# Kernel optimization log

Measured on AMD Instinct MI355X. Metric: run time of the kernel, lower is better.

The kernel has to match this reference:

```python
import jax, jax.numpy as jnp
import numpy as np

N = 100000        # nodes
E = 1600000       # edges (avg degree 16)
F_IN = 64         # num_node_features
NHID = 64         # args.nhid
NCLS = 16         # num_classes
K1 = 8            # Chebyshev order of conv1


def setup_inputs() -> dict:
    key = jax.random.key(0)
    k0, k1, k2, k3 = jax.random.split(key, 4)
    x = jax.random.normal(k0, (N, F_IN), dtype=jnp.float32)
    edge_index = jax.random.randint(k1, (2, E), 0, N, dtype=jnp.int32)
    # ChebConv params: K linear maps (no per-lin bias) + one shared bias
    W1 = jax.random.normal(k2, (K1, F_IN, NHID), dtype=jnp.float32) * (1.0 / np.sqrt(F_IN))
    b1 = jnp.zeros((NHID,), dtype=jnp.float32)
    W2 = jax.random.normal(k3, (1, NHID, NCLS), dtype=jnp.float32) * (1.0 / np.sqrt(NHID))
    b2 = jnp.zeros((NCLS,), dtype=jnp.float32)
    return {"x": x, "edge_index": edge_index, "W1": W1, "b1": b1, "W2": W2, "b2": b2}


def _cheb_norm(edge_index, num_nodes):
    # PyG ChebConv.__norm__ with normalization='sym', lambda_max=2.0, unit edge weights:
    # remove self loops; L_hat = 2L/lambda_max - I = -D^{-1/2} A D^{-1/2}, diag = 0.
    row, col = edge_index[0], edge_index[1]
    nonself = (row != col).astype(jnp.float32)
    deg = jax.ops.segment_sum(nonself, row, num_segments=num_nodes)
    dinv = jnp.where(deg > 0, jax.lax.rsqrt(jnp.maximum(deg, 1.0)), 0.0)
    norm = -dinv[row] * dinv[col] * nonself
    return row, col, norm


def reference(x, edge_index, W1, b1, W2, b2):
    row, col, norm = _cheb_norm(edge_index, N)

    def prop(h):  # L_hat @ h via gather + scatter-add, [N,F]
        return jax.ops.segment_sum(h[col] * norm[:, None], row, num_segments=N)

    # conv1: ChebConv K=8 recursion  Tx_k = 2*L_hat*Tx_{k-1} - Tx_{k-2}
    tx_prev = x
    out = x @ W1[0]
    tx = prop(x)
    out = out + tx @ W1[1]
    for k in range(2, K1):
        tx_new = 2.0 * prop(tx) - tx_prev
        out = out + tx_new @ W1[k]
        tx_prev, tx = tx, tx_new
    h = jax.nn.relu(out + b1)
    # dropout: identity (eval mode)
    # conv2: ChebConv K=1 -> just Tx_0 = h
    logits = h @ W2[0] + b2
    return jax.nn.softmax(logits, axis=1)
```

## Files before the change

kernel.cpp:

```cpp
#include <hip/hip_runtime.h>
#include <hip/hip_fp16.h>

#define N_NODES 100000
#define N_EDGES 1600000
#define F 64
#define NCLS 16
#define K1 8
#define BSH 9
#define NBK 196
#define BROWS 512
#define BKCAP 9216
#define EPB 4096

using f16x8 = __attribute__((ext_vector_type(8))) _Float16;
using f32x4 = __attribute__((ext_vector_type(4))) float;

__global__ __launch_bounds__(256) void k_bucketA(const int* __restrict__ ei,
                                                 int* __restrict__ gcur,
                                                 int2* __restrict__ bk) {
    __shared__ int cnt[4][256];
    __shared__ int wbase[4][256];
    int tid = threadIdx.x;
    int w = tid >> 6;
    for (int i = tid; i < 1024; i += 256) ((int*)cnt)[i] = 0;
    __syncthreads();
    int packed[16];
    int e0 = blockIdx.x * EPB;
#pragma unroll
    for (int u = 0; u < 16; u++) {
        int e = e0 + u * 256 + tid;
        packed[u] = -1;
        if (e < N_EDGES) {
            int r = ei[e], c = ei[N_EDGES + e];
            if (r != c) {
                int b = r >> BSH;
                int rank = atomicAdd(&cnt[w][b], 1);
                packed[u] = (rank << 8) | b;
            }
        }
    }
    __syncthreads();
    {
        int c0 = cnt[0][tid], c1 = cnt[1][tid], c2 = cnt[2][tid], c3 = cnt[3][tid];
        int tot = c0 + c1 + c2 + c3;
        int g = tot ? atomicAdd(&gcur[tid], tot) : 0;
        wbase[0][tid] = g;
        wbase[1][tid] = g + c0;
        wbase[2][tid] = g + c0 + c1;
        wbase[3][tid] = g + c0 + c1 + c2;
    }
    __syncthreads();
#pragma unroll
    for (int u = 0; u < 16; u++) {
        if (packed[u] >= 0) {
            int e = e0 + u * 256 + tid;
            int r = ei[e], c = ei[N_EDGES + e];
            int b = packed[u] & 255;
            int rank = packed[u] >> 8;
            bk[(size_t)b * BKCAP + wbase[w][b] + rank] = make_int2(r, c);
        }
    }
}

__global__ __launch_bounds__(256) void k_degB(const int2* __restrict__ bk,
                                              const int* __restrict__ gcur,
                                              int* __restrict__ deg,
                                              float* __restrict__ dinv) {
    __shared__ int hist[BROWS];
    int b = blockIdx.x;
    for (int i = threadIdx.x; i < BROWS; i += 256) hist[i] = 0;
    __syncthreads();
    int cnt = gcur[b];
    const int2* src = bk + (size_t)b * BKCAP;
    for (int i = threadIdx.x; i < cnt; i += 256)
        atomicAdd(&hist[src[i].x & (BROWS - 1)], 1);
    __syncthreads();
    int rbase = b << BSH;
    for (int i = threadIdx.x; i < BROWS; i += 256) {
        int gr = rbase + i;
        if (gr < N_NODES) {
            int d = hist[i];
            deg[gr] = d;
            dinv[gr] = d > 0 ? rsqrtf((float)d) : 0.f;
        }
    }
}

__global__ void k_scan1(const int* __restrict__ deg, int* __restrict__ rowptr, int* __restrict__ bsum) {
    __shared__ int sd[256];
    int tid = threadIdx.x;
    int base = blockIdx.x * 1024 + tid * 4;
    int v[4];
#pragma unroll
    for (int j = 0; j < 4; j++) {
        int idx = base + j;
        v[j] = (idx < N_NODES) ? deg[idx] : 0;
    }
    int s = v[0] + v[1] + v[2] + v[3];
    sd[tid] = s;
    __syncthreads();
    for (int d = 1; d < 256; d <<= 1) {
        int t = (tid >= d) ? sd[tid - d] : 0;
        __syncthreads();
        sd[tid] += t;
        __syncthreads();
    }
    int excl = sd[tid] - s;
    if (tid == 255) bsum[blockIdx.x] = sd[255];
    int run = excl;
#pragma unroll
    for (int j = 0; j < 4; j++) {
        int idx = base + j;
        if (idx < N_NODES) rowptr[idx] = run;
        run += v[j];
    }
}

__global__ void k_scan2(int* __restrict__ bsum, int* __restrict__ rowptr, int nblk) {
    if (threadIdx.x == 0 && blockIdx.x == 0) {
        int acc = 0;
        for (int b = 0; b < nblk; b++) { int t = bsum[b]; bsum[b] = acc; acc += t; }
        rowptr[N_NODES] = acc;
    }
}

__global__ void k_scan3(int* __restrict__ rowptr, const int* __restrict__ bsum) {
    int tid = threadIdx.x;
    int base = blockIdx.x * 1024 + tid * 4;
    int off = bsum[blockIdx.x];
#pragma unroll
    for (int j = 0; j < 4; j++) {
        int idx = base + j;
        if (idx < N_NODES) rowptr[idx] += off;
    }
}

__global__ __launch_bounds__(256) void k_fillB(const int2* __restrict__ bk,
                                               const int* __restrict__ gcur,
                                               const int* __restrict__ rowptr,
                                               const float* __restrict__ dinv,
                                               int2* __restrict__ csr_ew) {
    __shared__ int cur[BROWS];
    int b = blockIdx.x;
    for (int i = threadIdx.x; i < BROWS; i += 256) cur[i] = 0;
    __syncthreads();
    int cnt = gcur[b];
    const int2* src = bk + (size_t)b * BKCAP;
    for (int i = threadIdx.x; i < cnt; i += 256) {
        int2 rc = src[i];
        int rank = atomicAdd(&cur[rc.x & (BROWS - 1)], 1);
        float w = -dinv[rc.x] * dinv[rc.y];
        csr_ew[rowptr[rc.x] + rank] = make_int2(rc.y, __float_as_int(w));
    }
}

__global__ void k_cvt(const float* __restrict__ x, __half* __restrict__ t0) {
    int i = blockIdx.x * blockDim.x + threadIdx.x;
    int base = i * 4;
    if (base >= N_NODES * F) return;
    float4 v = *(const float4*)&x[base];
    __half2 a = __floats2half2_rn(v.x, v.y);
    __half2 b = __floats2half2_rn(v.z, v.w);
    *(__half2*)&t0[base] = a;
    *(__half2*)&t0[base + 2] = b;
}

__global__ void k_prepW(const float* __restrict__ W1, __half* __restrict__ Wf) {
    int t = blockIdx.x * blockDim.x + threadIdx.x;
    if (t >= K1 * 2 * 4 * 64) return;
    int lane = t & 63;
    int cb = (t >> 6) & 3;
    int fg = (t >> 8) & 1;
    int kidx = t >> 9;
    int col = cb * 16 + (lane & 15);
    int kbase = fg * 32 + (lane >> 4) * 8;
    f16x8 v;
#pragma unroll
    for (int j = 0; j < 8; j++)
        v[j] = (_Float16)W1[kidx * 4096 + (kbase + j) * 64 + col];
    *(f16x8*)(Wf + (size_t)t * 8) = v;
}

__global__ __launch_bounds__(256) void k_prop(const int* __restrict__ rowptr,
                                              const int2* __restrict__ csr_ew,
                                              const __half* __restrict__ src,
                                              const __half* __restrict__ prev,
                                              __half* __restrict__ dst,
                                              float alpha, float beta) {
    int wpair = (int)((blockIdx.x * blockDim.x + threadIdx.x) >> 6);
    int lane = threadIdx.x & 63;
    int nA = wpair * 2;
    if (nA >= N_NODES) return;
    int h = lane >> 5;
    int hl = lane & 31;
    int s3 = (lane >> 3) & 3;
    int fb = (lane & 7) * 8;
    int node = nA + h;
    bool valid = node < N_NODES;
    int cb  = valid ? rowptr[node] : 0;
    int end = valid ? rowptr[node + 1] : 0;

    float acc[8] = {};

    while (true) {
        int n_own = end - cb;
        if (n_own > 32) n_own = 32;
        if (n_own < 0) n_own = 0;
        int n_oth = __shfl(n_own, lane ^ 32, 64);
        int nmax = n_own > n_oth ? n_own : n_oth;
        if (nmax == 0) break;
        int2 e = make_int2(0, 0);
        if (hl < n_own) e = csr_ew[cb + hl];
        for (int j = 0; j < nmax; j += 16) {
            int cc[4];
            float ww[4];
#pragma unroll
            for (int g = 0; g < 4; g++) {
                int sl = (h << 5) | (j + g * 4 + s3);
                cc[g] = __shfl(e.x, sl, 64);
                ww[g] = __int_as_float(__shfl(e.y, sl, 64));
            }
            uint4 raw[4];
#pragma unroll
            for (int g = 0; g < 4; g++)
                raw[g] = *(const uint4*)(src + (size_t)cc[g] * F + fb);
#pragma unroll
            for (int g = 0; g < 4; g++) {
                float2 f0 = __half22float2(*(__half2*)&raw[g].x);
                float2 f1 = __half22float2(*(__half2*)&raw[g].y);
                float2 f2 = __half22float2(*(__half2*)&raw[g].z);
                float2 f3 = __half22float2(*(__half2*)&raw[g].w);
                acc[0] = fmaf(ww[g], f0.x, acc[0]);
                acc[1] = fmaf(ww[g], f0.y, acc[1]);
                acc[2] = fmaf(ww[g], f1.x, acc[2]);
                acc[3] = fmaf(ww[g], f1.y, acc[3]);
                acc[4] = fmaf(ww[g], f2.x, acc[4]);
                acc[5] = fmaf(ww[g], f2.y, acc[5]);
                acc[6] = fmaf(ww[g], f3.x, acc[6]);
                acc[7] = fmaf(ww[g], f3.y, acc[7]);
            }
        }
        cb += n_own;
    }

#pragma unroll
    for (int i = 0; i < 8; i++) {
        acc[i] += __shfl_xor(acc[i], 8, 64);
        acc[i] += __shfl_xor(acc[i], 16, 64);
    }

    if ((lane & 24) == 0 && valid) {
        float r[8];
#pragma unroll
        for (int i = 0; i < 8; i++) r[i] = alpha * acc[i];
        if (beta != 0.f) {
            uint4 pv = *(const uint4*)(prev + (size_t)node * F + fb);
            float2 p0 = __half22float2(*(__half2*)&pv.x);
            float2 p1 = __half22float2(*(__half2*)&pv.y);
            float2 p2 = __half22float2(*(__half2*)&pv.z);
            float2 p3 = __half22float2(*(__half2*)&pv.w);
            r[0] -= beta * p0.x; r[1] -= beta * p0.y;
            r[2] -= beta * p1.x; r[3] -= beta * p1.y;
            r[4] -= beta * p2.x; r[5] -= beta * p2.y;
            r[6] -= beta * p3.x; r[7] -= beta * p3.y;
        }
        uint4 outv;
        *(__half2*)&outv.x = __floats2half2_rn(r[0], r[1]);
        *(__half2*)&outv.y = __floats2half2_rn(r[2], r[3]);
        *(__half2*)&outv.z = __floats2half2_rn(r[4], r[5]);
        *(__half2*)&outv.w = __floats2half2_rn(r[6], r[7]);
        *(uint4*)(dst + (size_t)node * F + fb) = outv;
    }
}

__global__ __launch_bounds__(256) void k_fused_mfma(const __half* __restrict__ T,
                                                    const __half* __restrict__ Wf,
                                                    const float* __restrict__ b1,
                                                    const float* __restrict__ W2,
                                                    const float* __restrict__ b2,
                                                    float* __restrict__ y) {
    __shared__ float Ht[64][65];
    __shared__ float W2l[64 * 16];
    __shared__ float b2l[16];
    int tid = threadIdx.x;
    int lane = tid & 63;
    int w = tid >> 6;
    int ln15 = lane & 15;
    int lg = lane >> 4;
    int base = blockIdx.x * 64;

    for (int j = tid; j < 64 * 16; j += 256) W2l[j] = W2[j];
    if (tid < 16) b2l[tid] = b2[tid];

    int nd = base + (w << 4) + ln15;
    if (nd > N_NODES - 1) nd = N_NODES - 1;

    f32x4 acc0 = {0.f, 0.f, 0.f, 0.f};
    f32x4 acc1 = {0.f, 0.f, 0.f, 0.f};
    f32x4 acc2 = {0.f, 0.f, 0.f, 0.f};
    f32x4 acc3 = {0.f, 0.f, 0.f, 0.f};

    for (int s = 0; s < 16; s++) {
        int kidx = s >> 1;
        int fg = s & 1;
        f16x8 a = *(const f16x8*)(T + ((size_t)kidx * N_NODES + nd) * F + fg * 32 + lg * 8);
        const __half* wb = Wf + ((size_t)((kidx * 2 + fg) * 4) * 64 + lane) * 8;
        f16x8 b0 = *(const f16x8*)(wb);
        f16x8 b1f = *(const f16x8*)(wb + 64 * 8);
        f16x8 b2f = *(const f16x8*)(wb + 128 * 8);
        f16x8 b3f = *(const f16x8*)(wb + 192 * 8);
        acc0 = __builtin_amdgcn_mfma_f32_16x16x32_f16(a, b0, acc0, 0, 0, 0);
        acc1 = __builtin_amdgcn_mfma_f32_16x16x32_f16(a, b1f, acc1, 0, 0, 0);
        acc2 = __builtin_amdgcn_mfma_f32_16x16x32_f16(a, b2f, acc2, 0, 0, 0);
        acc3 = __builtin_amdgcn_mfma_f32_16x16x32_f16(a, b3f, acc3, 0, 0, 0);
    }

    int hrow = (w << 4) + (lg << 2);
    {
        float bb0 = b1[0 * 16 + ln15];
        float bb1 = b1[1 * 16 + ln15];
        float bb2 = b1[2 * 16 + ln15];
        float bb3 = b1[3 * 16 + ln15];
#pragma unroll
        for (int r = 0; r < 4; r++) {
            float h0 = acc0[r] + bb0;
            float h1 = acc1[r] + bb1;
            float h2 = acc2[r] + bb2;
            float h3 = acc3[r] + bb3;
            Ht[hrow + r][0 * 16 + ln15] = h0 > 0.f ? h0 : 0.f;
            Ht[hrow + r][1 * 16 + ln15] = h1 > 0.f ? h1 : 0.f;
            Ht[hrow + r][2 * 16 + ln15] = h2 > 0.f ? h2 : 0.f;
            Ht[hrow + r][3 * 16 + ln15] = h3 > 0.f ? h3 : 0.f;
        }
    }
    __syncthreads();

    int node = tid >> 2;
    int cg = tid & 3;
    int gnode = base + node;
    if (gnode >= N_NODES) return;
    float l0 = b2l[cg * 4 + 0], l1 = b2l[cg * 4 + 1], l2 = b2l[cg * 4 + 2], l3 = b2l[cg * 4 + 3];
    for (int f = 0; f < 64; f++) {
        float h = Ht[node][f];
        l0 = fmaf(h, W2l[f * 16 + cg * 4 + 0], l0);
        l1 = fmaf(h, W2l[f * 16 + cg * 4 + 1], l1);
        l2 = fmaf(h, W2l[f * 16 + cg * 4 + 2], l2);
        l3 = fmaf(h, W2l[f * 16 + cg * 4 + 3], l3);
    }
    float m = fmaxf(fmaxf(l0, l1), fmaxf(l2, l3));
    m = fmaxf(m, __shfl_xor(m, 1, 64));
    m = fmaxf(m, __shfl_xor(m, 2, 64));
    float e0 = expf(l0 - m), e1 = expf(l1 - m), e2 = expf(l2 - m), e3 = expf(l3 - m);
    float s = e0 + e1 + e2 + e3;
    s += __shfl_xor(s, 1, 64);
    s += __shfl_xor(s, 2, 64);
    float inv = 1.f / s;
    float4 o = make_float4(e0 * inv, e1 * inv, e2 * inv, e3 * inv);
    *(float4*)&y[(size_t)gnode * 16 + cg * 4] = o;
}


extern "C" void kernel_launch(void* const* d_in, const int* in_sizes, int n_in,
                              void* d_out, int out_size, void* d_ws, size_t ws_size,
                              hipStream_t stream) {
    const float* x  = (const float*)d_in[0];
    const int*   ei = (const int*)d_in[1];
    const float* W1 = (const float*)d_in[2];
    const float* b1 = (const float*)d_in[3];
    const float* W2 = (const float*)d_in[4];
    const float* b2 = (const float*)d_in[5];
    float* y = (float*)d_out;

    char* p = (char*)d_ws;
    auto alloc = [&](size_t bytes) {
        char* q = p;
        p += (bytes + 255) & ~(size_t)255;
        return q;
    };
    int*   deg    = (int*)alloc((size_t)N_NODES * 4);
    float* dinv   = (float*)alloc((size_t)N_NODES * 4);
    int*   rowptr = (int*)alloc((size_t)(N_NODES + 1) * 4);
    int*   bsum   = (int*)alloc(128 * 4);
    int*   gcur   = (int*)alloc(256 * 4);
    int2*  csr_ew = (int2*)alloc((size_t)N_EDGES * 8);
    __half* T     = (__half*)alloc((size_t)K1 * N_NODES * F * 2);
    __half* Wf    = (__half*)alloc((size_t)K1 * 2 * 4 * 64 * 8 * 2);

    int2* bk = (int2*)T;

    hipMemsetAsync(gcur, 0, 256 * 4, stream);

    k_bucketA<<<(N_EDGES + EPB - 1) / EPB, 256, 0, stream>>>(ei, gcur, bk);
    k_degB<<<NBK, 256, 0, stream>>>(bk, gcur, deg, dinv);
    int nblk = (N_NODES + 1023) / 1024;
    k_scan1<<<nblk, 256, 0, stream>>>(deg, rowptr, bsum);
    k_scan2<<<1, 64, 0, stream>>>(bsum, rowptr, nblk);
    k_scan3<<<nblk, 256, 0, stream>>>(rowptr, bsum);
    k_fillB<<<NBK, 256, 0, stream>>>(bk, gcur, rowptr, dinv, csr_ew);
    k_prepW<<<16, 256, 0, stream>>>(W1, Wf);

    const size_t TSZ = (size_t)N_NODES * F;
    __half* Tk[K1];
    for (int k = 0; k < K1; k++) Tk[k] = T + (size_t)k * TSZ;

    k_cvt<<<(N_NODES * F / 4 + 255) / 256, 256, 0, stream>>>(x, Tk[0]);

    int npair = (N_NODES + 1) / 2;
    int prop_blocks = (npair + 3) / 4;
    k_prop<<<prop_blocks, 256, 0, stream>>>(rowptr, csr_ew, Tk[0], Tk[0], Tk[1], 1.f, 0.f);
    for (int k = 2; k < K1; k++)
        k_prop<<<prop_blocks, 256, 0, stream>>>(rowptr, csr_ew, Tk[k - 1], Tk[k - 2], Tk[k], 2.f, 1.f);

    int gemm_blocks = (N_NODES + 63) / 64;
    k_fused_mfma<<<gemm_blocks, 256, 0, stream>>>(T, Wf, b1, W2, b2, y);
}
```

Before: 343.2 us.

## Fold row-pointer scan into per-bucket degree kernel and keep edge ids in registers

The three-kernel global prefix scan is replaced by a per-bucket local scan inside k_degB. Row pointers now point into a padded bucket-strided CSR (bucket base plus local offset), and k_prop reads each row's end from deg instead of rowptr[node+1]. The bucketing kernel also keeps row and column ids in registers rather than reloading them from global memory. This removes three small launches and a serial single-thread scan, at the cost of a larger, sparser csr_ew allocation with gaps between buckets.

New measurement: 324.6 us. -5.4%, faster.

```diff
diff --git a/kernel.cpp b/kernel.cpp
--- a/kernel.cpp
+++ b/kernel.cpp
@@ -24,16 +24,17 @@
     int w = tid >> 6;
     for (int i = tid; i < 1024; i += 256) ((int*)cnt)[i] = 0;
     __syncthreads();
-    int packed[16];
+    int rv[16], cv[16], packed[16];
     int e0 = blockIdx.x * EPB;
 #pragma unroll
     for (int u = 0; u < 16; u++) {
         int e = e0 + u * 256 + tid;
         packed[u] = -1;
         if (e < N_EDGES) {
-            int r = ei[e], c = ei[N_EDGES + e];
-            if (r != c) {
-                int b = r >> BSH;
+            rv[u] = ei[e];
+            cv[u] = ei[N_EDGES + e];
+            if (rv[u] != cv[u]) {
+                int b = rv[u] >> BSH;
                 int rank = atomicAdd(&cnt[w][b], 1);
                 packed[u] = (rank << 8) | b;
             }
@@ -53,11 +54,9 @@
 #pragma unroll
     for (int u = 0; u < 16; u++) {
         if (packed[u] >= 0) {
-            int e = e0 + u * 256 + tid;
-            int r = ei[e], c = ei[N_EDGES + e];
             int b = packed[u] & 255;
             int rank = packed[u] >> 8;
-            bk[(size_t)b * BKCAP + wbase[w][b] + rank] = make_int2(r, c);
+            bk[(size_t)b * BKCAP + wbase[w][b] + rank] = make_int2(rv[u], cv[u]);
         }
     }
 }
@@ -65,38 +64,21 @@
 __global__ __launch_bounds__(256) void k_degB(const int2* __restrict__ bk,
                                               const int* __restrict__ gcur,
                                               int* __restrict__ deg,
-                                              float* __restrict__ dinv) {
+                                              float* __restrict__ dinv,
+                                              int* __restrict__ rowptr) {
     __shared__ int hist[BROWS];
+    __shared__ int sd[256];
     int b = blockIdx.x;
-    for (int i = threadIdx.x; i < BROWS; i += 256) hist[i] = 0;
+    int tid = threadIdx.x;
+    for (int i = tid; i < BROWS; i += 256) hist[i] = 0;
     __syncthreads();
     int cnt = gcur[b];
     const int2* src = bk + (size_t)b * BKCAP;
-    for (int i = threadIdx.x; i < cnt; i += 256)
+    for (int i = tid; i < cnt; i += 256)
         atomicAdd(&hist[src[i].x & (BROWS - 1)], 1);
     __syncthreads();
-    int rbase = b << BSH;
-    for (int i = threadIdx.x; i < BROWS; i += 256) {
-        int gr = rbase + i;
-        if (gr < N_NODES) {
-            int d = hist[i];
-            deg[gr] = d;
-            dinv[gr] = d > 0 ? rsqrtf((float)d) : 0.f;
-        }
-    }
-}
-
-__global__ void k_scan1(const int* __restrict__ deg, int* __restrict__ rowptr, int* __restrict__ bsum) {
-    __shared__ int sd[256];
-    int tid = threadIdx.x;
-    int base = blockIdx.x * 1024 + tid * 4;
-    int v[4];
-#pragma unroll
-    for (int j = 0; j < 4; j++) {
-        int idx = base + j;
-        v[j] = (idx < N_NODES) ? deg[idx] : 0;
-    }
-    int s = v[0] + v[1] + v[2] + v[3];
+    int v0 = hist[2 * tid], v1 = hist[2 * tid + 1];
+    int s = v0 + v1;
     sd[tid] = s;
     __syncthreads();
     for (int d = 1; d < 256; d <<= 1) {
@@ -106,32 +88,19 @@
         __syncthreads();
     }
     int excl = sd[tid] - s;
-    if (tid == 255) bsum[blockIdx.x] = sd[255];
-    int run = excl;
-#pragma unroll
-    for (int j = 0; j < 4; j++) {
-        int idx = base + j;
-        if (idx < N_NODES) rowptr[idx] = run;
-        run += v[j];
-    }
-}
-
-__global__ void k_scan2(int* __restrict__ bsum, int* __restrict__ rowptr, int nblk) {
-    if (threadIdx.x == 0 && blockIdx.x == 0) {
-        int acc = 0;
-        for (int b = 0; b < nblk; b++) { int t = bsum[b]; bsum[b] = acc; acc += t; }
-        rowptr[N_NODES] = acc;
-    }
-}
-
-__global__ void k_scan3(int* __restrict__ rowptr, const int* __restrict__ bsum) {
-    int tid = threadIdx.x;
-    int base = blockIdx.x * 1024 + tid * 4;
-    int off = bsum[blockIdx.x];
-#pragma unroll
-    for (int j = 0; j < 4; j++) {
-        int idx = base + j;
-        if (idx < N_NODES) rowptr[idx] += off;
+    int rbase = b << BSH;
+    int cbase = b * BKCAP;
+    int gr0 = rbase + 2 * tid;
+    int gr1 = gr0 + 1;
+    if (gr0 < N_NODES) {
+        deg[gr0] = v0;
+        dinv[gr0] = v0 > 0 ? rsqrtf((float)v0) : 0.f;
+        rowptr[gr0] = cbase + excl;
+    }
+    if (gr1 < N_NODES) {
+        deg[gr1] = v1;
+        dinv[gr1] = v1 > 0 ? rsqrtf((float)v1) : 0.f;
+        rowptr[gr1] = cbase + excl + v0;
     }
 }
 
@@ -182,6 +151,7 @@
 }
 
 __global__ __launch_bounds__(256) void k_prop(const int* __restrict__ rowptr,
+                                              const int* __restrict__ deg,
                                               const int2* __restrict__ csr_ew,
                                               const __half* __restrict__ src,
                                               const __half* __restrict__ prev,
@@ -198,7 +168,7 @@
     int node = nA + h;
     bool valid = node < N_NODES;
     int cb  = valid ? rowptr[node] : 0;
-    int end = valid ? rowptr[node + 1] : 0;
+    int end = valid ? cb + deg[node] : 0;
 
     float acc[8] = {};
 
@@ -380,9 +350,8 @@
     int*   deg    = (int*)alloc((size_t)N_NODES * 4);
     float* dinv   = (float*)alloc((size_t)N_NODES * 4);
     int*   rowptr = (int*)alloc((size_t)(N_NODES + 1) * 4);
-    int*   bsum   = (int*)alloc(128 * 4);
     int*   gcur   = (int*)alloc(256 * 4);
-    int2*  csr_ew = (int2*)alloc((size_t)N_EDGES * 8);
+    int2*  csr_ew = (int2*)alloc((size_t)NBK * BKCAP * 8);
     __half* T     = (__half*)alloc((size_t)K1 * N_NODES * F * 2);
     __half* Wf    = (__half*)alloc((size_t)K1 * 2 * 4 * 64 * 8 * 2);
 
@@ -391,11 +360,7 @@
     hipMemsetAsync(gcur, 0, 256 * 4, stream);
 
     k_bucketA<<<(N_EDGES + EPB - 1) / EPB, 256, 0, stream>>>(ei, gcur, bk);
-    k_degB<<<NBK, 256, 0, stream>>>(bk, gcur, deg, dinv);
-    int nblk = (N_NODES + 1023) / 1024;
-    k_scan1<<<nblk, 256, 0, stream>>>(deg, rowptr, bsum);
-    k_scan2<<<1, 64, 0, stream>>>(bsum, rowptr, nblk);
-    k_scan3<<<nblk, 256, 0, stream>>>(rowptr, bsum);
+    k_degB<<<NBK, 256, 0, stream>>>(bk, gcur, deg, dinv, rowptr);
     k_fillB<<<NBK, 256, 0, stream>>>(bk, gcur, rowptr, dinv, csr_ew);
     k_prepW<<<16, 256, 0, stream>>>(W1, Wf);
 
@@ -407,9 +372,9 @@
 
     int npair = (N_NODES + 1) / 2;
     int prop_blocks = (npair + 3) / 4;
-    k_prop<<<prop_blocks, 256, 0, stream>>>(rowptr, csr_ew, Tk[0], Tk[0], Tk[1], 1.f, 0.f);
+    k_prop<<<prop_blocks, 256, 0, stream>>>(rowptr, deg, csr_ew, Tk[0], Tk[0], Tk[1], 1.f, 0.f);
     for (int k = 2; k < K1; k++)
-        k_prop<<<prop_blocks, 256, 0, stream>>>(rowptr, csr_ew, Tk[k - 1], Tk[k - 2], Tk[k], 2.f, 1.f);
+        k_prop<<<prop_blocks, 256, 0, stream>>>(rowptr, deg, csr_ew, Tk[k - 1], Tk[k - 2], Tk[k], 2.f, 1.f);
 
     int gemm_blocks = (N_NODES + 63) / 64;
     k_fused_mfma<<<gemm_blocks, 256, 0, stream>>>(T, Wf, b1, W2, b2, y);
```
